# Performance work log

Measured on AMD Instinct MI355X. Metric: run time of the kernel, lower is better.

The kernel has to match this reference:

```python
import jax, jax.numpy as jnp
import numpy as np

N_NODES = 50000
N_EDGES = 800000
HIDDEN = 128
N_GRAPHS = 32
EPS = 1e-5  # GraphNorm eps


def setup_inputs() -> dict:
    key = jax.random.key(0)
    ks = jax.random.split(key, 8)
    x = jax.random.normal(ks[0], (N_NODES, HIDDEN), dtype=jnp.float32)
    edge_index = jax.random.randint(ks[1], (2, N_EDGES), 0, N_NODES, dtype=jnp.int64)
    batch = jnp.sort(jax.random.randint(ks[2], (N_NODES,), 0, N_GRAPHS, dtype=jnp.int64))
    s = 1.0 / np.sqrt(HIDDEN)
    # SAGEConv: lin_l (applied to aggregated neighbors, with bias) and lin_r (root, no bias)
    W_l = jax.random.normal(ks[3], (HIDDEN, HIDDEN), dtype=jnp.float32) * s
    b_l = jnp.zeros((HIDDEN,), dtype=jnp.float32)
    W_r = jax.random.normal(ks[4], (HIDDEN, HIDDEN), dtype=jnp.float32) * s
    # GraphNorm params: weight, bias, mean_scale (alpha)
    gn_weight = jnp.ones((HIDDEN,), dtype=jnp.float32)
    gn_bias = jnp.zeros((HIDDEN,), dtype=jnp.float32)
    gn_mean_scale = jnp.ones((HIDDEN,), dtype=jnp.float32)
    return {
        "x": x, "edge_index": edge_index, "batch": batch,
        "W_l": W_l, "b_l": b_l, "W_r": W_r,
        "gn_weight": gn_weight, "gn_bias": gn_bias, "gn_mean_scale": gn_mean_scale,
    }


def reference(x, edge_index, batch, W_l, b_l, W_r, gn_weight, gn_bias, gn_mean_scale):
    src, dst = edge_index[0], edge_index[1]
    n = x.shape[0]
    # --- SAGEConv: mean aggregation of source features at destination ---
    msg_sum = jax.ops.segment_sum(x[src], dst, num_segments=n)          # [N, D]
    deg = jax.ops.segment_sum(jnp.ones((src.shape[0],), x.dtype), dst, num_segments=n)
    agg = msg_sum / jnp.maximum(deg, 1.0)[:, None]
    out = agg @ W_l + b_l + x @ W_r                                      # [N, D]
    # --- GraphNorm: per-graph mean/var with learnable mean scale alpha ---
    g_cnt = jax.ops.segment_sum(jnp.ones((n,), x.dtype), batch, num_segments=N_GRAPHS)[:, None]
    g_cnt = jnp.maximum(g_cnt, 1.0)
    mean = jax.ops.segment_sum(out, batch, num_segments=N_GRAPHS) / g_cnt  # [G, D]
    sub = out - gn_mean_scale * mean[batch]
    var = jax.ops.segment_sum(sub * sub, batch, num_segments=N_GRAPHS) / g_cnt
    normed = gn_weight * sub / jnp.sqrt(var[batch] + EPS) + gn_bias
    # --- exact GELU (torch nn.GELU default), dropout = identity (eval), residual ---
    return jax.nn.gelu(normed, approximate=False) + x
```

## Files before the change

kernel.cpp:

```cpp
#include <hip/hip_runtime.h>
#include <math.h>

#define NN 50000
#define NE 800000
#define HD 128
#define NG 32
#define GN_EPS 1e-5f
#define NSH 8

#define NBLK_R 800
#define CH_R   1000
#define NBUCK  196
#define NBB    (NBUCK * NBLK_R)
#define NCHS   ((NBB + 255) / 256)
#define DCAP   8192
#define PREP_BLKS 3125

typedef __bf16 v8bf __attribute__((ext_vector_type(8)));
typedef float f32x4 __attribute__((ext_vector_type(4)));

#define ROWPTR_OFF 0
#define BB_OFF     50016
#define CS_OFF     206816
#define GSUMS_OFF  207840
#define GSQS_OFF   240608
#define GCNTS_OFF  273376
#define MEAN_OFF   273632
#define RSTD_OFF   277728
#define SRCS_OFF   281824
#define PSRC_OFF   681824
#define PDLOW_OFF  1081824
#define WPACK_OFF  1281824
#define ABUF_OFF   1298208
#define MEMSET_INTS (32768 + 32768 + 256)

__device__ __forceinline__ unsigned short f2bf(float f) {
  unsigned int u = __float_as_uint(f);
  u = (u + 0x7fffu + ((u >> 16) & 1u)) >> 16;
  return (unsigned short)u;
}
__device__ __forceinline__ float bf_lo(unsigned int u) { return __uint_as_float(u << 16); }
__device__ __forceinline__ float bf_hi(unsigned int u) { return __uint_as_float(u & 0xffff0000u); }

__global__ __launch_bounds__(256) void prep_rhist_k(const float* __restrict__ x,
    const float* __restrict__ Wl, const float* __restrict__ Wr,
    unsigned short* __restrict__ Abuf, unsigned short* __restrict__ wp,
    int* __restrict__ zbase, const int* __restrict__ ei, int* __restrict__ bb) {
  __shared__ int h[NBUCK];
  int tid = threadIdx.x;
  if (blockIdx.x < PREP_BLKS) {
    int i = blockIdx.x * 256 + tid;
    if (i < MEMSET_INTS) zbase[i] = 0;
    if (i < 32768) {
      int e = i & 7, lane = (i >> 3) & 63, nt = (i >> 9) & 7, ks = i >> 12;
      int k = ks * 32 + (lane >> 4) * 8 + e;
      int c = nt * 16 + (lane & 15);
      float v = (k < HD) ? Wl[k * HD + c] : Wr[(k - HD) * HD + c];
      wp[i] = f2bf(v);
    }
    if (i < NN * 16) {
      int n = i >> 4, seg = i & 15;
      const float* src = x + (size_t)n * HD + seg * 8;
      float4 v0 = *(const float4*)(src);
      float4 v1 = *(const float4*)(src + 4);
      uint4 o;
      o.x = (unsigned)f2bf(v0.x) | ((unsigned)f2bf(v0.y) << 16);
      o.y = (unsigned)f2bf(v0.z) | ((unsigned)f2bf(v0.w) << 16);
      o.z = (unsigned)f2bf(v1.x) | ((unsigned)f2bf(v1.y) << 16);
      o.w = (unsigned)f2bf(v1.z) | ((unsigned)f2bf(v1.w) << 16);
      *(uint4*)(Abuf + (size_t)n * 256 + 128 + seg * 8) = o;
    }
  } else {
    int b = blockIdx.x - PREP_BLKS;
    for (int i = tid; i < NBUCK; i += 256) h[i] = 0;
    __syncthreads();
    int base = b * CH_R;
    if (tid < CH_R / 4) {
      int4 d = *(const int4*)(ei + NE + base + tid * 4);
      atomicAdd(&h[d.x >> 8], 1);
      atomicAdd(&h[d.y >> 8], 1);
      atomicAdd(&h[d.z >> 8], 1);
      atomicAdd(&h[d.w >> 8], 1);
    }
    __syncthreads();
    for (int i = tid; i < NBUCK; i += 256) bb[i * NBLK_R + b] = h[i];
  }
}

__global__ __launch_bounds__(256) void csum_k(const int* __restrict__ bb,
                                              int* __restrict__ cs) {
  __shared__ int red[4];
  int i = blockIdx.x * 256 + threadIdx.x;
  int v = (i < NBB) ? bb[i] : 0;
#pragma unroll
  for (int off = 32; off; off >>= 1) v += __shfl_down(v, off, 64);
  if ((threadIdx.x & 63) == 0) red[threadIdx.x >> 6] = v;
  __syncthreads();
  if (threadIdx.x == 0) cs[blockIdx.x] = red[0] + red[1] + red[2] + red[3];
}

__global__ __launch_bounds__(1024) void cscan_k(int* __restrict__ cs) {
  __shared__ int s[1024];
  int t = threadIdx.x;
  int v = (t < NCHS) ? cs[t] : 0;
  s[t] = v;
  __syncthreads();
  for (int off = 1; off < 1024; off <<= 1) {
    int u = (t >= off) ? s[t - off] : 0;
    __syncthreads();
    s[t] += u;
    __syncthreads();
  }
  if (t < NCHS) cs[t] = s[t] - v;
}

__global__ __launch_bounds__(256) void cfill_k(int* __restrict__ bb,
                                               const int* __restrict__ cs) {
  __shared__ int s[256];
  int t = threadIdx.x;
  int i = blockIdx.x * 256 + t;
  int c = (i < NBB) ? bb[i] : 0;
  s[t] = c;
  __syncthreads();
#pragma unroll
  for (int off = 1; off < 256; off <<= 1) {
    int u = (t >= off) ? s[t - off] : 0;
    __syncthreads();
    s[t] += u;
    __syncthreads();
  }
  if (i < NBB) bb[i] = cs[blockIdx.x] + s[t] - c;
}

__global__ __launch_bounds__(256) void rscatter_k(const int* __restrict__ ei,
    const int* __restrict__ bb, unsigned short* __restrict__ psrc,
    unsigned char* __restrict__ pdlow) {
  __shared__ int cur[NBUCK];
  int tid = threadIdx.x, b = blockIdx.x;
  for (int i = tid; i < NBUCK; i += 256) cur[i] = bb[i * NBLK_R + b];
  __syncthreads();
  int base = b * CH_R;
  if (tid < CH_R / 4) {
    int4 s4 = *(const int4*)(ei + base + tid * 4);
    int4 d4 = *(const int4*)(ei + NE + base + tid * 4);
    int p;
    p = atomicAdd(&cur[d4.x >> 8], 1); psrc[p] = (unsigned short)s4.x; pdlow[p] = (unsigned char)(d4.x & 255);
    p = atomicAdd(&cur[d4.y >> 8], 1); psrc[p] = (unsigned short)s4.y; pdlow[p] = (unsigned char)(d4.y & 255);
    p = atomicAdd(&cur[d4.z >> 8], 1); psrc[p] = (unsigned short)s4.z; pdlow[p] = (unsigned char)(d4.z & 255);
    p = atomicAdd(&cur[d4.w >> 8], 1); psrc[p] = (unsigned short)s4.w; pdlow[p] = (unsigned char)(d4.w & 255);
  }
}

__global__ __launch_bounds__(256) void rfinal_k(const int* __restrict__ bb,
    const unsigned short* __restrict__ psrc, const unsigned char* __restrict__ pdlow,
    unsigned short* __restrict__ srcs, int* __restrict__ rowptr) {
  __shared__ unsigned short ssrc[DCAP];
  __shared__ unsigned short sout[DCAP];
  __shared__ unsigned char sdl[DCAP];
  __shared__ int h2[256], scn[256], cur2[256];
  int tid = threadIdx.x, k = blockIdx.x;
  int segB = bb[k * NBLK_R];
  int segE = (k == NBUCK - 1) ? NE : bb[(k + 1) * NBLK_R];
  int cnt = segE - segB;
  for (int j = tid; j < cnt; j += 256) {
    ssrc[j] = psrc[segB + j];
    sdl[j] = pdlow[segB + j];
  }
  h2[tid] = 0;
  __syncthreads();
  for (int j = tid; j < cnt; j += 256) atomicAdd(&h2[sdl[j]], 1);
  __syncthreads();
  scn[tid] = h2[tid];
  __syncthreads();
#pragma unroll
  for (int off = 1; off < 256; off <<= 1) {
    int u = (tid >= off) ? scn[tid - off] : 0;
    __syncthreads();
    scn[tid] += u;
    __syncthreads();
  }
  int excl = scn[tid] - h2[tid];
  cur2[tid] = excl;
  int dst = k * 256 + tid;
  if (dst < NN) rowptr[dst] = segB + excl;
  if (dst == NN - 1) rowptr[NN] = NE;
  __syncthreads();
  for (int j = tid; j < cnt; j += 256) {
    int p = atomicAdd(&cur2[sdl[j]], 1);
    sout[p] = ssrc[j];
  }
  __syncthreads();
  for (int j = tid; j < cnt; j += 256) srcs[segB + j] = sout[j];
}

__global__ __launch_bounds__(256) void gather_k(const int* __restrict__ rowptr,
    const unsigned short* __restrict__ srcs, unsigned short* Abuf) {
  int t = blockIdx.x * 256 + threadIdx.x;
  int n = t >> 4, q = t & 15;
  if (n >= NN) return;
  int b = rowptr[n], e = rowptr[n + 1];
  float a0=0,a1=0,a2=0,a3=0,a4=0,a5=0,a6=0,a7=0;
  int i = b;
  for (; i + 1 < e; i += 2) {
    int s0 = srcs[i], s1 = srcs[i + 1];
    uint4 v0 = *(const uint4*)(Abuf + (size_t)s0 * 256 + 128 + q * 8);
    uint4 v1 = *(const uint4*)(Abuf + (size_t)s1 * 256 + 128 + q * 8);
    a0 += bf_lo(v0.x) + bf_lo(v1.x);  a1 += bf_hi(v0.x) + bf_hi(v1.x);
    a2 += bf_lo(v0.y) + bf_lo(v1.y);  a3 += bf_hi(v0.y) + bf_hi(v1.y);
    a4 += bf_lo(v0.z) + bf_lo(v1.z);  a5 += bf_hi(v0.z) + bf_hi(v1.z);
    a6 += bf_lo(v0.w) + bf_lo(v1.w);  a7 += bf_hi(v0.w) + bf_hi(v1.w);
  }
  if (i < e) {
    int s0 = srcs[i];
    uint4 v0 = *(const uint4*)(Abuf + (size_t)s0 * 256 + 128 + q * 8);
    a0 += bf_lo(v0.x); a1 += bf_hi(v0.x);
    a2 += bf_lo(v0.y); a3 += bf_hi(v0.y);
    a4 += bf_lo(v0.z); a5 += bf_hi(v0.z);
    a6 += bf_lo(v0.w); a7 += bf_hi(v0.w);
  }
  float inv = 1.0f / fmaxf((float)(e - b), 1.0f);
  uint4 o;
  o.x = (unsigned)f2bf(a0 * inv) | ((unsigned)f2bf(a1 * inv) << 16);
  o.y = (unsigned)f2bf(a2 * inv) | ((unsigned)f2bf(a3 * inv) << 16);
  o.z = (unsigned)f2bf(a4 * inv) | ((unsigned)f2bf(a5 * inv) << 16);
  o.w = (unsigned)f2bf(a6 * inv) | ((unsigned)f2bf(a7 * inv) << 16);
  *(uint4*)(Abuf + (size_t)n * 256 + q * 8) = o;
}

__global__ __launch_bounds__(256) void gemm_k(const unsigned short* __restrict__ Abuf,
    const unsigned short* __restrict__ wp, const float* __restrict__ bl,
    const int* __restrict__ batch, float* __restrict__ out,
    float* __restrict__ gsumS, float* __restrict__ gsqS,
    float* __restrict__ gcntS) {
  __shared__ float lsum[16][136];
  __shared__ float lsq[16][136];
  __shared__ unsigned char ridx[64];
  __shared__ int sg0, snrun;
  int tid = threadIdx.x;
  int base0 = blockIdx.x * 64;
  int nvalid = min(64, NN - base0);
  if (tid == 0) {
    int g0 = batch[base0];
    sg0 = g0;
    snrun = batch[base0 + nvalid - 1] - g0 + 1;
  }
  __syncthreads();
  if (tid < 64)
    ridx[tid] = (tid < nvalid) ? (unsigned char)(batch[base0 + tid] - sg0)
                               : (unsigned char)0;
  __syncthreads();

  int shard = blockIdx.x & 7;
  float* gs = gsumS + shard * (NG * HD);
  float* gq = gsqS + shard * (NG * HD);
  float* gc = gcntS + shard * NG;

  int wave = tid >> 6;
  int lane = tid & 63;
  int base = base0 + wave * 16;
  int row = lane & 15, kg = lane >> 4;
  int node = base + row;
  if (node > NN - 1) node = NN - 1;
  const unsigned short* arow = Abuf + (size_t)node * 256 + kg * 8;
  f32x4 acc[8] = {};
#pragma unroll
  for (int ks = 0; ks < 8; ++ks) {
    v8bf a = __builtin_bit_cast(v8bf, *(const uint4*)(arow + ks * 32));
    const unsigned short* wrow = wp + ks * 4096 + lane * 8;
#pragma unroll
    for (int nt = 0; nt < 8; ++nt) {
      v8bf b = __builtin_bit_cast(v8bf, *(const uint4*)(wrow + nt * 512));
      acc[nt] = __builtin_amdgcn_mfma_f32_16x16x32_bf16(a, b, acc[nt], 0, 0, 0);
    }
  }
  int c0 = lane & 15;
  float bv[8];
#pragma unroll
  for (int nt = 0; nt < 8; ++nt) bv[nt] = bl[nt * 16 + c0];

  if (snrun == 1) {
    float ps0[8] = {}, pq0[8] = {};
#pragma unroll
    for (int j = 0; j < 4; ++j) {
      int n = base0 + wave * 16 + kg * 4 + j;
      if (n >= NN) break;
      float* orow = out + (size_t)n * HD;
#pragma unroll
      for (int nt = 0; nt < 8; ++nt) {
        float v = acc[nt][j] + bv[nt];
        orow[nt * 16 + c0] = v;
        ps0[nt] += v;
        pq0[nt] += v * v;
      }
    }
    int r = wave * 4 + kg;
#pragma unroll
    for (int nt = 0; nt < 8; ++nt) {
      lsum[r][nt * 16 + c0] = ps0[nt];
      lsq[r][nt * 16 + c0] = pq0[nt];
    }
    __syncthreads();
    if (tid < HD) {
      float s = 0.0f, q = 0.0f;
#pragma unroll
      for (int r2 = 0; r2 < 16; ++r2) { s += lsum[r2][tid]; q += lsq[r2][tid]; }
      atomicAdd(gs + sg0 * HD + tid, s);
      atomicAdd(gq + sg0 * HD + tid, q);
    }
    if (tid == 0) atomicAdd(gc + sg0, (float)nvalid);
  } else if (snrun == 2) {
    float ps0[8] = {}, pq0[8] = {}, ps1[8] = {}, pq1[8] = {};
#pragma unroll
    for (int j = 0; j < 4; ++j) {
      int rb = wave * 16 + kg * 4 + j;
      int n = base0 + rb;
      if (n >= NN) break;
      float* orow = out + (size_t)n * HD;
      bool b1 = (ridx[rb] != 0);
#pragma unroll
      for (int nt = 0; nt < 8; ++nt) {
        float v = acc[nt][j] + bv[nt];
        orow[nt * 16 + c0] = v;
        if (b1) { ps1[nt] += v; pq1[nt] += v * v; }
        else    { ps0[nt] += v; pq0[nt] += v * v; }
      }
    }
    int r = wave * 4 + kg;
#pragma unroll
    for (int nt = 0; nt < 8; ++nt) {
      lsum[r][nt * 16 + c0] = ps0[nt];
      lsq[r][nt * 16 + c0] = pq0[nt];
    }
    __syncthreads();
    if (tid < HD) {
      float s = 0.0f, q = 0.0f;
#pragma unroll
      for (int r2 = 0; r2 < 16; ++r2) { s += lsum[r2][tid]; q += lsq[r2][tid]; }
      atomicAdd(gs + sg0 * HD + tid, s);
      atomicAdd(gq + sg0 * HD + tid, q);
    }
    __syncthreads();
#pragma unroll
    for (int nt = 0; nt < 8; ++nt) {
      lsum[r][nt * 16 + c0] = ps1[nt];
      lsq[r][nt * 16 + c0] = pq1[nt];
    }
    __syncthreads();
    if (tid < HD) {
      float s = 0.0f, q = 0.0f;
#pragma unroll
      for (int r2 = 0; r2 < 16; ++r2) { s += lsum[r2][tid]; q += lsq[r2][tid]; }
      atomicAdd(gs + (sg0 + 1) * HD + tid, s);
      atomicAdd(gq + (sg0 + 1) * HD + tid, q);
    }
    if (tid == 0) {
      int n0 = 0;
      for (int r2 = 0; r2 < nvalid; ++r2) n0 += (ridx[r2] == 0);
      atomicAdd(gc + sg0, (float)n0);
      atomicAdd(gc + sg0 + 1, (float)(nvalid - n0));
    }
  } else {
#pragma unroll
    for (int j = 0; j < 4; ++j) {
      int rb = wave * 16 + kg * 4 + j;
      int n = base0 + rb;
      if (n >= NN) break;
      float* orow = out + (size_t)n * HD;
      int g = sg0 + ridx[rb];
#pragma unroll
      for (int nt = 0; nt < 8; ++nt) {
        float v = acc[nt][j] + bv[nt];
        orow[nt * 16 + c0] = v;
        atomicAdd(gs + g * HD + nt * 16 + c0, v);
        atomicAdd(gq + g * HD + nt * 16 + c0, v * v);
      }
    }
    if (tid < nvalid) atomicAdd(gc + batch[base0 + tid], 1.0f);
  }
}

__global__ __launch_bounds__(256) void finalize_k(const float* __restrict__ gsumS,
    const float* __restrict__ gsqS, const float* __restrict__ gcntS,
    const float* __restrict__ alpha, float* __restrict__ mean,
    float* __restrict__ rstd) {
  int i = blockIdx.x * 256 + threadIdx.x;
  if (i >= NG * HD) return;
  int g = i >> 7, d = i & 127;
  float s = 0.0f, q = 0.0f, cnt = 0.0f;
#pragma unroll
  for (int sh = 0; sh < NSH; ++sh) {
    s += gsumS[sh * (NG * HD) + i];
    q += gsqS[sh * (NG * HD) + i];
    cnt += gcntS[sh * NG + g];
  }
  cnt = fmaxf(cnt, 1.0f);
  float mu = s / cnt;
  float a = alpha[d];
  float var = q / cnt - mu * mu * (2.0f * a - a * a);
  mean[i] = mu;
  rstd[i] = rsqrtf(fmaxf(var, 0.0f) + GN_EPS);
}

__global__ __launch_bounds__(256) void final_k(float* __restrict__ out,
    const float* __restrict__ x, const int* __restrict__ batch,
    const float* __restrict__ mean, const float* __restrict__ rstd,
    const float* __restrict__ alpha, const float* __restrict__ gw,
    const float* __restrict__ gb) {
  size_t i = ((size_t)blockIdx.x * 256 + threadIdx.x) * 4;
  if (i >= (size_t)NN * HD) return;
  int n = (int)(i >> 7);
  int d = (int)(i & 127);
  int g = batch[n];
  float4 v  = *(float4*)(out + i);
  float4 xv = *(const float4*)(x + i);
  float4 al = *(const float4*)(alpha + d);
  float4 w  = *(const float4*)(gw + d);
  float4 b  = *(const float4*)(gb + d);
  float4 mn = *(const float4*)(mean + (size_t)g * HD + d);
  float4 rs = *(const float4*)(rstd + (size_t)g * HD + d);
  float vv[4] = {v.x, v.y, v.z, v.w};
  float xx[4] = {xv.x, xv.y, xv.z, xv.w};
  float aa[4] = {al.x, al.y, al.z, al.w};
  float ww[4] = {w.x, w.y, w.z, w.w};
  float bb2[4] = {b.x, b.y, b.z, b.w};
  float mm[4] = {mn.x, mn.y, mn.z, mn.w};
  float rr[4] = {rs.x, rs.y, rs.z, rs.w};
  float r[4];
#pragma unroll
  for (int c = 0; c < 4; ++c) {
    float sub = vv[c] - aa[c] * mm[c];
    float nm  = ww[c] * sub * rr[c] + bb2[c];
    float ge  = 0.5f * nm * (1.0f + erff(nm * 0.70710678118654752f));
    r[c] = ge + xx[c];
  }
  float4 res = {r[0], r[1], r[2], r[3]};
  *(float4*)(out + i) = res;
}

extern "C" void kernel_launch(void* const* d_in, const int* in_sizes, int n_in,
                              void* d_out, int out_size, void* d_ws, size_t ws_size,
                              hipStream_t stream) {
  const float* x     = (const float*)d_in[0];
  const int*   ei    = (const int*)d_in[1];
  const int*   batch = (const int*)d_in[2];
  const float* Wl    = (const float*)d_in[3];
  const float* bl    = (const float*)d_in[4];
  const float* Wr    = (const float*)d_in[5];
  const float* gw    = (const float*)d_in[6];
  const float* gb    = (const float*)d_in[7];
  const float* alpha = (const float*)d_in[8];

  float* out = (float*)d_out;
  int*   wsi = (int*)d_ws;
  float* wsf = (float*)d_ws;
  int* rowptr = wsi + ROWPTR_OFF;
  int* bb     = wsi + BB_OFF;
  int* cs     = wsi + CS_OFF;
  float* gsumS = wsf + GSUMS_OFF;
  float* gsqS  = wsf + GSQS_OFF;
  float* gcntS = wsf + GCNTS_OFF;
  float* mean  = wsf + MEAN_OFF;
  float* rstd  = wsf + RSTD_OFF;
  unsigned short* srcs  = (unsigned short*)(wsi + SRCS_OFF);
  unsigned short* psrc  = (unsigned short*)(wsi + PSRC_OFF);
  unsigned char*  pdlow = (unsigned char*)(wsi + PDLOW_OFF);
  unsigned short* wpack = (unsigned short*)(wsi + WPACK_OFF);
  unsigned short* Abuf  = (unsigned short*)(wsi + ABUF_OFF);

  prep_rhist_k<<<PREP_BLKS + NBLK_R, 256, 0, stream>>>(
      x, Wl, Wr, Abuf, wpack, (int*)(wsf + GSUMS_OFF), ei, bb);

  csum_k<<<NCHS, 256, 0, stream>>>(bb, cs);
  cscan_k<<<1, 1024, 0, stream>>>(cs);
  cfill_k<<<NCHS, 256, 0, stream>>>(bb, cs);
  rscatter_k<<<NBLK_R, 256, 0, stream>>>(ei, bb, psrc, pdlow);
  rfinal_k<<<NBUCK, 256, 0, stream>>>(bb, psrc, pdlow, srcs, rowptr);

  gather_k<<<(NN * 16 + 255) / 256, 256, 0, stream>>>(rowptr, srcs, Abuf);

  gemm_k<<<(NN + 63) / 64, 256, 0, stream>>>(Abuf, wpack, bl, batch, out,
                                             gsumS, gsqS, gcntS);

  finalize_k<<<16, 256, 0, stream>>>(gsumS, gsqS, gcntS, alpha, mean, rstd);

  final_k<<<(NN * HD / 4 + 255) / 256, 256, 0, stream>>>(
      out, x, batch, mean, rstd, alpha, gw, gb);
}
```

Before: 103.2 us.

## Store GEMM output as bf16, fold chunk scan into fill, enlarge radix chunks

The GEMM now writes its pre-norm output as a bf16 intermediate buffer instead of fp32 into the output array, and final_k reads it back. This halves the traffic for that round trip but rounds the values before normalization. Radix-sort chunks grow from 1000 to 3200 edges (250 blocks), so the chunk-prefix array fits in 256 entries. The separate single-block scan kernel is removed by having every cfill block redundantly scan the chunk sums, which saves one launch.

```diff
diff --git a/kernel.cpp b/kernel.cpp
--- a/kernel.cpp
+++ b/kernel.cpp
@@ -8,8 +8,8 @@
 #define GN_EPS 1e-5f
 #define NSH 8
 
-#define NBLK_R 800
-#define CH_R   1000
+#define NBLK_R 250
+#define CH_R   3200
 #define NBUCK  196
 #define NBB    (NBUCK * NBLK_R)
 #define NCHS   ((NBB + 255) / 256)
@@ -21,17 +21,18 @@
 
 #define ROWPTR_OFF 0
 #define BB_OFF     50016
-#define CS_OFF     206816
-#define GSUMS_OFF  207840
-#define GSQS_OFF   240608
-#define GCNTS_OFF  273376
-#define MEAN_OFF   273632
-#define RSTD_OFF   277728
-#define SRCS_OFF   281824
-#define PSRC_OFF   681824
-#define PDLOW_OFF  1081824
-#define WPACK_OFF  1281824
-#define ABUF_OFF   1298208
+#define CS_OFF     99016
+#define GSUMS_OFF  99280
+#define GSQS_OFF   132048
+#define GCNTS_OFF  164816
+#define MEAN_OFF   165072
+#define RSTD_OFF   169168
+#define SRCS_OFF   173264
+#define PSRC_OFF   573264
+#define PDLOW_OFF  973264
+#define WPACK_OFF  1173264
+#define ABUF_OFF   1189648
+#define OBF_OFF    7589648
 #define MEMSET_INTS (32768 + 32768 + 256)
 
 __device__ __forceinline__ unsigned short f2bf(float f) {
@@ -75,8 +76,8 @@
     for (int i = tid; i < NBUCK; i += 256) h[i] = 0;
     __syncthreads();
     int base = b * CH_R;
-    if (tid < CH_R / 4) {
-      int4 d = *(const int4*)(ei + NE + base + tid * 4);
+    for (int j = tid; j < CH_R / 4; j += 256) {
+      int4 d = *(const int4*)(ei + NE + base + j * 4);
       atomicAdd(&h[d.x >> 8], 1);
       atomicAdd(&h[d.y >> 8], 1);
       atomicAdd(&h[d.z >> 8], 1);
@@ -99,37 +100,27 @@
   if (threadIdx.x == 0) cs[blockIdx.x] = red[0] + red[1] + red[2] + red[3];
 }
 
-__global__ __launch_bounds__(1024) void cscan_k(int* __restrict__ cs) {
-  __shared__ int s[1024];
-  int t = threadIdx.x;
-  int v = (t < NCHS) ? cs[t] : 0;
-  s[t] = v;
-  __syncthreads();
-  for (int off = 1; off < 1024; off <<= 1) {
-    int u = (t >= off) ? s[t - off] : 0;
-    __syncthreads();
-    s[t] += u;
-    __syncthreads();
-  }
-  if (t < NCHS) cs[t] = s[t] - v;
-}
-
 __global__ __launch_bounds__(256) void cfill_k(int* __restrict__ bb,
                                                const int* __restrict__ cs) {
+  __shared__ int sb[256];
   __shared__ int s[256];
   int t = threadIdx.x;
+  sb[t] = (t < NCHS) ? cs[t] : 0;
   int i = blockIdx.x * 256 + t;
   int c = (i < NBB) ? bb[i] : 0;
   s[t] = c;
   __syncthreads();
 #pragma unroll
   for (int off = 1; off < 256; off <<= 1) {
-    int u = (t >= off) ? s[t - off] : 0;
-    __syncthreads();
-    s[t] += u;
-    __syncthreads();
-  }
-  if (i < NBB) bb[i] = cs[blockIdx.x] + s[t] - c;
+    int u1 = (t >= off) ? sb[t - off] : 0;
+    int u2 = (t >= off) ? s[t - off] : 0;
+    __syncthreads();
+    sb[t] += u1;
+    s[t] += u2;
+    __syncthreads();
+  }
+  int chunkpre = (blockIdx.x == 0) ? 0 : sb[blockIdx.x - 1];
+  if (i < NBB) bb[i] = chunkpre + s[t] - c;
 }
 
 __global__ __launch_bounds__(256) void rscatter_k(const int* __restrict__ ei,
@@ -140,9 +131,9 @@
   for (int i = tid; i < NBUCK; i += 256) cur[i] = bb[i * NBLK_R + b];
   __syncthreads();
   int base = b * CH_R;
-  if (tid < CH_R / 4) {
-    int4 s4 = *(const int4*)(ei + base + tid * 4);
-    int4 d4 = *(const int4*)(ei + NE + base + tid * 4);
+  for (int j = tid; j < CH_R / 4; j += 256) {
+    int4 s4 = *(const int4*)(ei + base + j * 4);
+    int4 d4 = *(const int4*)(ei + NE + base + j * 4);
     int p;
     p = atomicAdd(&cur[d4.x >> 8], 1); psrc[p] = (unsigned short)s4.x; pdlow[p] = (unsigned char)(d4.x & 255);
     p = atomicAdd(&cur[d4.y >> 8], 1); psrc[p] = (unsigned short)s4.y; pdlow[p] = (unsigned char)(d4.y & 255);
@@ -229,7 +220,7 @@
 
 __global__ __launch_bounds__(256) void gemm_k(const unsigned short* __restrict__ Abuf,
     const unsigned short* __restrict__ wp, const float* __restrict__ bl,
-    const int* __restrict__ batch, float* __restrict__ out,
+    const int* __restrict__ batch, unsigned short* __restrict__ obf,
     float* __restrict__ gsumS, float* __restrict__ gsqS,
     float* __restrict__ gcntS) {
   __shared__ float lsum[16][136];
@@ -284,11 +275,11 @@
     for (int j = 0; j < 4; ++j) {
       int n = base0 + wave * 16 + kg * 4 + j;
       if (n >= NN) break;
-      float* orow = out + (size_t)n * HD;
+      unsigned short* orow = obf + (size_t)n * HD;
 #pragma unroll
       for (int nt = 0; nt < 8; ++nt) {
         float v = acc[nt][j] + bv[nt];
-        orow[nt * 16 + c0] = v;
+        orow[nt * 16 + c0] = f2bf(v);
         ps0[nt] += v;
         pq0[nt] += v * v;
       }
@@ -315,12 +306,12 @@
       int rb = wave * 16 + kg * 4 + j;
       int n = base0 + rb;
       if (n >= NN) break;
-      float* orow = out + (size_t)n * HD;
+      unsigned short* orow = obf + (size_t)n * HD;
       bool b1 = (ridx[rb] != 0);
 #pragma unroll
       for (int nt = 0; nt < 8; ++nt) {
         float v = acc[nt][j] + bv[nt];
-        orow[nt * 16 + c0] = v;
+        orow[nt * 16 + c0] = f2bf(v);
         if (b1) { ps1[nt] += v; pq1[nt] += v * v; }
         else    { ps0[nt] += v; pq0[nt] += v * v; }
       }
@@ -365,12 +356,12 @@
       int rb = wave * 16 + kg * 4 + j;
       int n = base0 + rb;
       if (n >= NN) break;
-      float* orow = out + (size_t)n * HD;
+      unsigned short* orow = obf + (size_t)n * HD;
       int g = sg0 + ridx[rb];
 #pragma unroll
       for (int nt = 0; nt < 8; ++nt) {
         float v = acc[nt][j] + bv[nt];
-        orow[nt * 16 + c0] = v;
+        orow[nt * 16 + c0] = f2bf(v);
         atomicAdd(gs + g * HD + nt * 16 + c0, v);
         atomicAdd(gq + g * HD + nt * 16 + c0, v * v);
       }
@@ -401,24 +392,24 @@
   rstd[i] = rsqrtf(fmaxf(var, 0.0f) + GN_EPS);
 }
 
-__global__ __launch_bounds__(256) void final_k(float* __restrict__ out,
-    const float* __restrict__ x, const int* __restrict__ batch,
-    const float* __restrict__ mean, const float* __restrict__ rstd,
-    const float* __restrict__ alpha, const float* __restrict__ gw,
-    const float* __restrict__ gb) {
+__global__ __launch_bounds__(256) void final_k(const unsigned short* __restrict__ obf,
+    float* __restrict__ out, const float* __restrict__ x,
+    const int* __restrict__ batch, const float* __restrict__ mean,
+    const float* __restrict__ rstd, const float* __restrict__ alpha,
+    const float* __restrict__ gw, const float* __restrict__ gb) {
   size_t i = ((size_t)blockIdx.x * 256 + threadIdx.x) * 4;
   if (i >= (size_t)NN * HD) return;
   int n = (int)(i >> 7);
   int d = (int)(i & 127);
   int g = batch[n];
-  float4 v  = *(float4*)(out + i);
+  uint2 ov = *(const uint2*)(obf + i);
   float4 xv = *(const float4*)(x + i);
   float4 al = *(const float4*)(alpha + d);
   float4 w  = *(const float4*)(gw + d);
   float4 b  = *(const float4*)(gb + d);
   float4 mn = *(const float4*)(mean + (size_t)g * HD + d);
   float4 rs = *(const float4*)(rstd + (size_t)g * HD + d);
-  float vv[4] = {v.x, v.y, v.z, v.w};
+  float vv[4] = {bf_lo(ov.x), bf_hi(ov.x), bf_lo(ov.y), bf_hi(ov.y)};
   float xx[4] = {xv.x, xv.y, xv.z, xv.w};
   float aa[4] = {al.x, al.y, al.z, al.w};
   float ww[4] = {w.x, w.y, w.z, w.w};
@@ -466,23 +457,23 @@
   unsigned char*  pdlow = (unsigned char*)(wsi + PDLOW_OFF);
   unsigned short* wpack = (unsigned short*)(wsi + WPACK_OFF);
   unsigned short* Abuf  = (unsigned short*)(wsi + ABUF_OFF);
+  unsigned short* obf   = (unsigned short*)(wsi + OBF_OFF);
 
   prep_rhist_k<<<PREP_BLKS + NBLK_R, 256, 0, stream>>>(
       x, Wl, Wr, Abuf, wpack, (int*)(wsf + GSUMS_OFF), ei, bb);
 
   csum_k<<<NCHS, 256, 0, stream>>>(bb, cs);
-  cscan_k<<<1, 1024, 0, stream>>>(cs);
   cfill_k<<<NCHS, 256, 0, stream>>>(bb, cs);
   rscatter_k<<<NBLK_R, 256, 0, stream>>>(ei, bb, psrc, pdlow);
   rfinal_k<<<NBUCK, 256, 0, stream>>>(bb, psrc, pdlow, srcs, rowptr);
 
   gather_k<<<(NN * 16 + 255) / 256, 256, 0, stream>>>(rowptr, srcs, Abuf);
 
-  gemm_k<<<(NN + 63) / 64, 256, 0, stream>>>(Abuf, wpack, bl, batch, out,
+  gemm_k<<<(NN + 63) / 64, 256, 0, stream>>>(Abuf, wpack, bl, batch, obf,
                                              gsumS, gsqS, gcntS);
 
   finalize_k<<<16, 256, 0, stream>>>(gsumS, gsqS, gcntS, alpha, mean, rstd);
 
   final_k<<<(NN * HD / 4 + 255) / 256, 256, 0, stream>>>(
-      out, x, batch, mean, rstd, alpha, gw, gb);
-}
+      obf, out, x, batch, mean, rstd, alpha, gw, gb);
+}
```

Result: slower. 108.4 us (+5.0%).
